# Kernel tuning notes

Measured on AMD Instinct MI355X. Metric: run time of the kernel, lower is better.

## Reference

```python
import jax, jax.numpy as jnp
import numpy as np
from functools import partial

H = 512
V = 32000


def setup_inputs() -> dict:
    key = jax.random.key(0)
    ks = jax.random.split(key, 16)
    B, Td, Te = 16, 64, 64
    s = 0.02
    inp = {
        'input_seqs': jax.random.normal(ks[0], (B, Td, H), jnp.float32),
        'input_lengths': jax.random.randint(ks[1], (B,), 1, Td + 1, jnp.int32),
        'encoder_outputs': jax.random.normal(ks[2], (B, Te, H), jnp.float32),
        'encoder_length': jax.random.randint(ks[3], (B,), 1, Te + 1, jnp.int32),
        # GRU (1 layer, batch_first): PyTorch layout W_ih (3H,H), W_hh (3H,H)
        'W_ih': jax.random.normal(ks[4], (3 * H, H), jnp.float32) * s,
        'W_hh': jax.random.normal(ks[5], (3 * H, H), jnp.float32) * s,
        'b_ih': jnp.zeros((3 * H,), jnp.float32),
        'b_hh': jnp.zeros((3 * H,), jnp.float32),
        # Attn: W: Linear(2H -> H), v: Linear(H -> 1)
        'W_attn': jax.random.normal(ks[6], (H, 2 * H), jnp.float32) * s,
        'b_attn': jnp.zeros((H,), jnp.float32),
        'v_w': jax.random.normal(ks[7], (H,), jnp.float32) * s,
        'v_b': jnp.zeros((), jnp.float32),
        # dense: Linear(2H -> H), output: Linear(H -> V)
        'W_dense': jax.random.normal(ks[8], (H, 2 * H), jnp.float32) * s,
        'b_dense': jnp.zeros((H,), jnp.float32),
        'W_out': jax.random.normal(ks[9], (V, H), jnp.float32) * s,
        'b_out': jnp.zeros((V,), jnp.float32),
    }
    return inp


def gru_forward(x, lengths, W_ih, W_hh, b_ih, b_hh):
    # Emulates pack_padded_sequence + GRU + pad_packed_sequence:
    # hidden state frozen past each sequence's length, outputs zero there.
    B, T, Hd = x.shape
    x_proj = jnp.einsum('bth,gh->btg', x, W_ih) + b_ih  # (B,T,3H)

    def step(h, inp):
        xp, t = inp  # xp: (B,3H)
        hp = h @ W_hh.T + b_hh
        xr, xz, xn = jnp.split(xp, 3, axis=-1)
        hr, hz, hn = jnp.split(hp, 3, axis=-1)
        r = jax.nn.sigmoid(xr + hr)
        z = jax.nn.sigmoid(xz + hz)
        n = jnp.tanh(xn + r * hn)
        h_new = (1.0 - z) * n + z * h
        valid = (t < lengths)[:, None]
        h_keep = jnp.where(valid, h_new, h)
        y = jnp.where(valid, h_new, 0.0)
        return h_keep, y

    h0 = jnp.zeros((B, Hd), x.dtype)
    h_last, ys = jax.lax.scan(step, h0, (x_proj.swapaxes(0, 1), jnp.arange(T)))
    return ys.swapaxes(0, 1), h_last  # (B,T,H), (B,H)


def attn_forward(enc, dec, enc_len, dec_len, W_attn, b_attn, v_w, v_b):
    B, Te, Hd = enc.shape
    Td = dec.shape[1]
    e_mask = (jnp.arange(Te) < enc_len[:, None])  # (B,Te)
    d_mask = (jnp.arange(Td) < dec_len[:, None])  # (B,Td)
    mask = (d_mask[:, :, None] & e_mask[:, None, :]).astype(enc.dtype)  # (B,Td,Te)
    # split W on the concat axis: cat(enc,dec) @ W.T = enc@We.T + dec@Wd.T
    We, Wd = W_attn[:, :Hd], W_attn[:, Hd:]
    enc_p = jnp.einsum('beh,gh->beg', enc, We)  # (B,Te,H)
    dec_p = jnp.einsum('bdh,gh->bdg', dec, Wd)  # (B,Td,H)
    m4 = mask[..., None]
    # masked-then-projected, matching enc_outputs*mask / dec_outputs*mask in torch
    score = jnp.tanh(enc_p[:, None, :, :] * m4 + dec_p[:, :, None, :] * m4 + b_attn)  # (B,Td,Te,H)
    energy = jnp.einsum('bdeh,h->bde', score, v_w) + v_b  # (B,Td,Te)
    a = jax.nn.softmax(energy, axis=2)  # softmax over ALL Te incl. masked (faithful)
    a_m = a * mask
    s = a_m.sum(axis=2)
    s = jnp.where(s == 0, 1.0, s)
    attention = a_m / s[:, :, None]  # (B,Td,Te)
    # attention is already zero where mask==0, so enc*mask == plain enc here
    context = jnp.einsum('bde,beh->bdh', attention, enc)
    return context  # dropout is identity at eval


def reference(input_seqs, input_lengths, encoder_outputs, encoder_length,
              W_ih, W_hh, b_ih, b_hh, W_attn, b_attn, v_w, v_b,
              W_dense, b_dense, W_out, b_out):
    dec_out, h_last = gru_forward(input_seqs, input_lengths, W_ih, W_hh, b_ih, b_hh)
    context = attn_forward(encoder_outputs, dec_out, encoder_length, input_lengths,
                           W_attn, b_attn, v_w, v_b)
    outputs = jnp.concatenate((dec_out, context), axis=2)  # (B,Td,2H)
    dense = jnp.tanh(jnp.einsum('bdg,hg->bdh', outputs, W_dense) + b_dense)
    logits = jnp.einsum('bdh,vh->bdv', dense, W_out) + b_out  # (B,Td,V)
    return logits, h_last[None]  # hidden: (n_layers=1, B, H)
```

## Files before the change

### kernel.cpp

```cpp
#include <hip/hip_runtime.h>
#include <stdint.h>


#define Hdim 512
#define Vdim 32000
#define Bdim 16
#define Tdim 64
#define BT   1024
#define GANG_BLOCKS 16

typedef __attribute__((ext_vector_type(8))) short bf16x8;
typedef __attribute__((ext_vector_type(4))) float f32x4;

static __device__ __forceinline__ unsigned short f2bf(float f) {
    unsigned u = __float_as_uint(f);
    u = u + 0x7FFFu + ((u >> 16) & 1u);
    return (unsigned short)(u >> 16);
}
static __device__ __forceinline__ float bf2f(unsigned short h) {
    return __uint_as_float((unsigned)h << 16);
}
static __device__ __forceinline__ float fast_tanh(float x) {
    return 2.f / (1.f + __expf(-2.f * x)) - 1.f;
}


#define U_ZERO 8320
#define U_INP  131072
#define U_WIH  196608
#define U_WAT  131072
#define U_WDE  131072
#define U_ENC  131072
#define U_SPLIT (U_INP + U_WIH + U_WAT + U_WDE + U_ENC)
#define U_WOUT 4096000
#define U_TOT  (U_ZERO + U_SPLIT + U_WOUT)

__global__ __launch_bounds__(256) void preproc_kernel(
    const float* __restrict__ input_seqs,
    const float* __restrict__ W_ih,
    const float* __restrict__ W_attn,
    const float* __restrict__ W_dense,
    const float* __restrict__ enc,
    const float* __restrict__ W_out,
    float* __restrict__ zero_base,
    unsigned short* __restrict__ inp_h, unsigned short* __restrict__ inp_l,
    unsigned short* __restrict__ Wih_h, unsigned short* __restrict__ Wih_l,
    unsigned short* __restrict__ Wat_h, unsigned short* __restrict__ Wat_l,
    unsigned short* __restrict__ Wde_h, unsigned short* __restrict__ Wde_l,
    unsigned short* __restrict__ enc_h, unsigned short* __restrict__ enc_l,
    unsigned short* __restrict__ Wout_bf)
{
    int u = blockIdx.x * 256 + threadIdx.x;
    const int stride = gridDim.x * 256;
    for (; u < U_TOT; u += stride) {
        int r = u;
        if (r < U_ZERO) {
            float4 z; z.x = 0.f; z.y = 0.f; z.z = 0.f; z.w = 0.f;
            *(float4*)(zero_base + r * 4) = z;
            continue;
        }
        r -= U_ZERO;
        if (r >= U_SPLIT) {
            int i = (r - U_SPLIT) * 4;
            float4 v = *(const float4*)(W_out + i);
            unsigned short h[4] = {f2bf(v.x), f2bf(v.y), f2bf(v.z), f2bf(v.w)};
            *(uint2*)(Wout_bf + i) = *(const uint2*)h;
            continue;
        }
        const float* src; unsigned short* hi; unsigned short* lo;
        if (r < U_INP) { src = input_seqs; hi = inp_h; lo = inp_l; }
        else { r -= U_INP;
            if (r < U_WIH) { src = W_ih; hi = Wih_h; lo = Wih_l; }
            else { r -= U_WIH;
                if (r < U_WAT) { src = W_attn; hi = Wat_h; lo = Wat_l; }
                else { r -= U_WAT;
                    if (r < U_WDE) { src = W_dense; hi = Wde_h; lo = Wde_l; }
                    else { r -= U_WDE; src = enc; hi = enc_h; lo = enc_l; }
                }
            }
        }
        int i = r * 4;
        float4 v = *(const float4*)(src + i);
        float f[4] = {v.x, v.y, v.z, v.w};
        unsigned short h[4], l[4];
#pragma unroll
        for (int k = 0; k < 4; ++k) {
            h[k] = f2bf(f[k]);
            l[k] = f2bf(f[k] - bf2f(h[k]));
        }
        *(uint2*)(hi + i) = *(const uint2*)h;
        *(uint2*)(lo + i) = *(const uint2*)l;
    }
}


struct GemmSmem {
    unsigned short AsH[128 * 40];
    unsigned short AsL[128 * 40];
    unsigned short BsH[128 * 40];
    unsigned short BsL[128 * 40];
};

static __device__ __forceinline__ void gemm_tile(
    GemmSmem& S, int m0, int n0,
    const unsigned short* __restrict__ Ah, const unsigned short* __restrict__ Al, int lda,
    const unsigned short* __restrict__ Bh, const unsigned short* __restrict__ Bl, int ldb,
    const float* __restrict__ bias,
    float* __restrict__ C, unsigned short* __restrict__ Cb, int ldc,
    int K, int act)
{
    const int tid = threadIdx.x;
    const int wave = tid >> 6, lane = tid & 63;
    const int wm = (wave >> 1) * 64, wn = (wave & 1) * 64;
    const int lrow = lane & 15, lk = (lane >> 4) * 8;

    f32x4 acc[4][4];
#pragma unroll
    for (int i = 0; i < 4; ++i)
#pragma unroll
        for (int j = 0; j < 4; ++j) acc[i][j] = (f32x4){0.f, 0.f, 0.f, 0.f};

    for (int k0 = 0; k0 < K; k0 += 32) {
#pragma unroll
        for (int i = 0; i < 2; ++i) {
            int idx = tid + i * 256;
            int rr = idx >> 2, kq = (idx & 3) * 8;
            size_t ao = (size_t)(m0 + rr) * lda + k0 + kq;
            size_t bo = (size_t)(n0 + rr) * ldb + k0 + kq;
            *(uint4*)(&S.AsH[rr * 40 + kq]) = *(const uint4*)(Ah + ao);
            *(uint4*)(&S.AsL[rr * 40 + kq]) = *(const uint4*)(Al + ao);
            *(uint4*)(&S.BsH[rr * 40 + kq]) = *(const uint4*)(Bh + bo);
            *(uint4*)(&S.BsL[rr * 40 + kq]) = *(const uint4*)(Bl + bo);
        }
        __syncthreads();
        bf16x8 ah[4], al[4], bh[4], bl[4];
#pragma unroll
        for (int i = 0; i < 4; ++i) {
            ah[i] = *(const bf16x8*)(&S.AsH[(wm + i * 16 + lrow) * 40 + lk]);
            al[i] = *(const bf16x8*)(&S.AsL[(wm + i * 16 + lrow) * 40 + lk]);
        }
#pragma unroll
        for (int j = 0; j < 4; ++j) {
            bh[j] = *(const bf16x8*)(&S.BsH[(wn + j * 16 + lrow) * 40 + lk]);
            bl[j] = *(const bf16x8*)(&S.BsL[(wn + j * 16 + lrow) * 40 + lk]);
        }
#pragma unroll
        for (int i = 0; i < 4; ++i)
#pragma unroll
            for (int j = 0; j < 4; ++j) {
                acc[i][j] = __builtin_amdgcn_mfma_f32_16x16x32_bf16(ah[i], bh[j], acc[i][j], 0, 0, 0);
                acc[i][j] = __builtin_amdgcn_mfma_f32_16x16x32_bf16(ah[i], bl[j], acc[i][j], 0, 0, 0);
                acc[i][j] = __builtin_amdgcn_mfma_f32_16x16x32_bf16(al[i], bh[j], acc[i][j], 0, 0, 0);
            }
        __syncthreads();
    }

    const int crow = m0 + wm + ((lane >> 4) * 4);
    const int ccol = n0 + wn + (lane & 15);
#pragma unroll
    for (int i = 0; i < 4; ++i) {
#pragma unroll
        for (int j = 0; j < 4; ++j) {
            int col = ccol + j * 16;
            float bv = bias[col];
#pragma unroll
            for (int rr = 0; rr < 4; ++rr) {
                int row = crow + i * 16 + rr;
                float v = acc[i][j][rr] + bv;
                if (act == 1) v = fast_tanh(v);
                if (Cb) Cb[(size_t)row * ldc + col] = f2bf(v);
                else    C [(size_t)row * ldc + col] = v;
            }
        }
    }
}

__global__ __launch_bounds__(256) void gemm_split(
    const unsigned short* __restrict__ Ah, const unsigned short* __restrict__ Al, int lda,
    const unsigned short* __restrict__ Bh, const unsigned short* __restrict__ Bl, int ldb,
    const float* __restrict__ bias,
    float* __restrict__ C, unsigned short* __restrict__ Cb, int ldc,
    int K, int act)
{
    __shared__ GemmSmem S;
    gemm_tile(S, blockIdx.y * 128, blockIdx.x * 128,
              Ah, Al, lda, Bh, Bl, ldb, bias, C, Cb, ldc, K, act);
}

__global__ __launch_bounds__(256) void gemm_split_dual(
    const unsigned short* __restrict__ A0h, const unsigned short* __restrict__ A0l,
    const unsigned short* __restrict__ B0h, const unsigned short* __restrict__ B0l,
    const float* __restrict__ bias0, float* __restrict__ C0,
    const unsigned short* __restrict__ A1h, const unsigned short* __restrict__ A1l,
    const unsigned short* __restrict__ B1h, const unsigned short* __restrict__ B1l,
    const float* __restrict__ bias1, float* __restrict__ C1)
{
    __shared__ GemmSmem S;
    const int bid = blockIdx.x;
    if (bid < 96) {
        gemm_tile(S, (bid / 12) * 128, (bid % 12) * 128,
                  A0h, A0l, Hdim, B0h, B0l, Hdim, bias0, C0, nullptr, 1536, Hdim, 0);
    } else {
        int r = bid - 96;
        gemm_tile(S, (r / 4) * 128, (r % 4) * 128,
                  A1h, A1l, Hdim, B1h, B1l, 1024, bias1, C1, nullptr, Hdim, Hdim, 0);
    }
}


__global__ __launch_bounds__(512) void gru_persistent(
    const float* __restrict__ xp,
    const float* __restrict__ Whh,
    const float* __restrict__ bhh,
    const int*   __restrict__ lengths,
    unsigned long long* __restrict__ hslots,
    unsigned short* __restrict__ cath,
    unsigned short* __restrict__ catl,
    float* __restrict__ h_last)
{
    const int bid  = blockIdx.x;
    const int b    = bid >> 4;
    const int blk  = bid & 15;
    const int tid  = threadIdx.x;
    const int wave = tid >> 6, lane = tid & 63;
    const int j0 = blk * 32 + wave * 4;
    const int k0 = lane * 8;

    __shared__ float hl[2][512];
    __shared__ unsigned short yh_buf[64][32];
    __shared__ unsigned short yl_buf[64][32];

    float w[12][8];
#pragma unroll
    for (int g = 0; g < 3; ++g)
#pragma unroll
        for (int jj = 0; jj < 4; ++jj) {
            const float* src = Whh + (size_t)(g * 512 + j0 + jj) * Hdim + k0;
            float4 a = *(const float4*)src;
            float4 bq = *(const float4*)(src + 4);
            int r = g * 4 + jj;
            w[r][0] = a.x;  w[r][1] = a.y;  w[r][2] = a.z;  w[r][3] = a.w;
            w[r][4] = bq.x; w[r][5] = bq.y; w[r][6] = bq.z; w[r][7] = bq.w;
        }

    const int j = j0 + (lane & 3);
    float bh_r = 0.f, bh_z = 0.f, bh_n = 0.f;
    if (lane < 4) {
        bh_r = bhh[j]; bh_z = bhh[512 + j]; bh_n = bhh[1024 + j];
    }
    const int len_b = lengths[b];
    float hprev = 0.f;

    const size_t PSTR = (size_t)Bdim * Hdim;
    unsigned long long* gslot = hslots + (size_t)b * Hdim;
    const float* xbase = xp + (size_t)b * Tdim * 1536;

    for (int t = 0; t < Tdim; ++t) {
        const int par = t & 1;

        float xr = 0.f, xz = 0.f, xn = 0.f;
        if (lane < 4) {
            const float* xrow = xbase + (size_t)t * 1536;
            xr = xrow[j]; xz = xrow[512 + j]; xn = xrow[1024 + j];
        }

        if (wave == 0) {
            const unsigned long long* sl = gslot + (size_t)par * PSTR + k0;
            unsigned long long v[8];
            bool ok;
            do {
#pragma unroll
                for (int q = 0; q < 8; ++q)
                    v[q] = __hip_atomic_load(sl + q, __ATOMIC_RELAXED,
                                             __HIP_MEMORY_SCOPE_AGENT);
                ok = true;
#pragma unroll
                for (int q = 0; q < 8; ++q)
                    ok = ok && ((unsigned)(v[q] >> 32) == (unsigned)t);
            } while (!ok);
#pragma unroll
            for (int q = 0; q < 8; ++q)
                hl[par][q * 64 + lane] = __uint_as_float((unsigned)v[q]);
        }
        __syncthreads();

        float hv[8];
#pragma unroll
        for (int q = 0; q < 8; ++q) hv[q] = hl[par][q * 64 + lane];

        float p[12];
#pragma unroll
        for (int r = 0; r < 12; ++r) {
            float s = 0.f;
#pragma unroll
            for (int k = 0; k < 8; ++k) s += w[r][k] * hv[k];
            p[r] = s;
        }

#pragma unroll
        for (int off = 1; off < 64; off <<= 1)
#pragma unroll
            for (int r = 0; r < 12; ++r)
                p[r] += __shfl_xor(p[r], off);

        if (lane < 4) {
            const int jj = lane;
            float hr = p[jj]     + bh_r;
            float hz = p[4 + jj] + bh_z;
            float hn = p[8 + jj] + bh_n;
            float rg = 1.f / (1.f + __expf(-(xr + hr)));
            float zg = 1.f / (1.f + __expf(-(xz + hz)));
            float ng = fast_tanh(xn + rg * hn);
            float hnew = (1.f - zg) * ng + zg * hprev;
            bool valid = t < len_b;
            float hkeep = valid ? hnew : hprev;
            hprev = hkeep;
            if (t < Tdim - 1) {
                unsigned long long pv =
                    ((unsigned long long)(unsigned)(t + 1) << 32) |
                    (unsigned long long)__float_as_uint(hkeep);
                __hip_atomic_store(gslot + (size_t)((t + 1) & 1) * PSTR + j, pv,
                                   __ATOMIC_RELAXED, __HIP_MEMORY_SCOPE_AGENT);
            } else {
                h_last[b * Hdim + j] = hkeep;
            }
            float y = valid ? hnew : 0.f;
            unsigned short yh = f2bf(y);
            yh_buf[t][wave * 4 + jj] = yh;
            yl_buf[t][wave * 4 + jj] = f2bf(y - bf2f(yh));
        }
    }

    __syncthreads();
    for (int idx = tid; idx < 64 * 16; idx += 512) {
        int t = idx >> 4, c = (idx & 15) * 2;
        size_t off = (size_t)(b * Tdim + t) * 1024 + blk * 32 + c;
        *(unsigned*)(cath + off) = *(const unsigned*)(&yh_buf[t][c]);
        *(unsigned*)(catl + off) = *(const unsigned*)(&yl_buf[t][c]);
    }
}


__global__ __launch_bounds__(256) void attn_kernel(
    const float* __restrict__ encp,
    const float* __restrict__ decp,
    const float* __restrict__ enc,
    const float* __restrict__ battn,
    const float* __restrict__ vw,
    const float* __restrict__ vb,
    const int* __restrict__ enc_len,
    const int* __restrict__ dec_len,
    unsigned short* __restrict__ cath,
    unsigned short* __restrict__ catl)
{
    const int blk = blockIdx.x;
    const int b = blk >> 6, d = blk & 63;
    const int tid = threadIdx.x;
    const size_t obase = (size_t)(b * Tdim + d) * 1024 + 512;

    if (d >= dec_len[b]) {
        for (int h = tid; h < Hdim; h += 256) { cath[obase + h] = 0; catl[obase + h] = 0; }
        return;
    }
    const int Tv = enc_len[b];

    __shared__ float dpb[512];
    __shared__ float vwl[512];
    __shared__ float part[64][4];
    __shared__ float a_lds[64];

    if (tid < 128) {
        const float4* dp4 = (const float4*)(decp + (size_t)(b * Tdim + d) * Hdim);
        float4 dv = dp4[tid];
        float4 bb = ((const float4*)battn)[tid];
        float4 r; r.x = dv.x + bb.x; r.y = dv.y + bb.y;
        r.z = dv.z + bb.z; r.w = dv.w + bb.w;
        ((float4*)dpb)[tid] = r;
        ((float4*)vwl)[tid] = ((const float4*)vw)[tid];
    }
    __syncthreads();

    const int e = tid >> 2, p = tid & 3;
    float s = 0.f;
    if (e < Tv) {
        const float4* ep4 = (const float4*)(encp + (size_t)(b * Tdim + e) * Hdim);
        const int q0 = p * 32;
        for (int q = q0; q < q0 + 32; ++q) {
            float4 ev = ep4[q];
            s += vwl[q * 4 + 0] * fast_tanh(ev.x + dpb[q * 4 + 0]);
            s += vwl[q * 4 + 1] * fast_tanh(ev.y + dpb[q * 4 + 1]);
            s += vwl[q * 4 + 2] * fast_tanh(ev.z + dpb[q * 4 + 2]);
            s += vwl[q * 4 + 3] * fast_tanh(ev.w + dpb[q * 4 + 3]);
        }
    }
    part[e][p] = s;
    __syncthreads();

    if (tid < 64) {
        const int e2 = tid;
        float en = (e2 < Tv) ? (part[e2][0] + part[e2][1] + part[e2][2] + part[e2][3] + vb[0]) : -1e30f;
        float m = en;
#pragma unroll
        for (int off = 32; off; off >>= 1) m = fmaxf(m, __shfl_xor(m, off));
        float ex = (e2 < Tv) ? __expf(en - m) : 0.f;
        float sum = ex;
#pragma unroll
        for (int off = 32; off; off >>= 1) sum += __shfl_xor(sum, off);
        a_lds[e2] = ex / sum;
    }
    __syncthreads();

    const int h = tid * 2;
    float c0 = 0.f, c1 = 0.f;
    for (int e3 = 0; e3 < Tv; ++e3) {
        float a = a_lds[e3];
        float2 ev = *(const float2*)(enc + (size_t)(b * Tdim + e3) * Hdim + h);
        c0 += a * ev.x; c1 += a * ev.y;
    }
    unsigned short h0 = f2bf(c0), h1 = f2bf(c1);
    cath[obase + h]     = h0;  catl[obase + h]     = f2bf(c0 - bf2f(h0));
    cath[obase + h + 1] = h1;  catl[obase + h + 1] = f2bf(c1 - bf2f(h1));
}


__global__ __launch_bounds__(512) void gemm_logits(
    const unsigned short* __restrict__ A,
    const unsigned short* __restrict__ B,
    const float* __restrict__ bias,
    float* __restrict__ C)
{
    const int K = Hdim;
    __shared__ unsigned short As[256 * 40];
    __shared__ unsigned short Bs[128 * 40];
    const int tid = threadIdx.x;
    const int m0 = blockIdx.y * 256, n0 = blockIdx.x * 128;
    const int wave = tid >> 6, lane = tid & 63;
    const int wm = (wave >> 1) * 64, wn = (wave & 1) * 64;
    const int lrow = lane & 15, lk = (lane >> 4) * 8;

    f32x4 acc[4][4];
#pragma unroll
    for (int i = 0; i < 4; ++i)
#pragma unroll
        for (int j = 0; j < 4; ++j) acc[i][j] = (f32x4){0.f, 0.f, 0.f, 0.f};

    for (int k0 = 0; k0 < K; k0 += 32) {
#pragma unroll
        for (int i = 0; i < 2; ++i) {
            int idx = tid + i * 512;
            int rr = idx >> 2, kq = (idx & 3) * 8;
            *(uint4*)(&As[rr * 40 + kq]) = *(const uint4*)(A + (size_t)(m0 + rr) * K + k0 + kq);
        }
        {
            int rr = tid >> 2, kq = (tid & 3) * 8;
            *(uint4*)(&Bs[rr * 40 + kq]) = *(const uint4*)(B + (size_t)(n0 + rr) * K + k0 + kq);
        }
        __syncthreads();
        bf16x8 af[4], bf[4];
#pragma unroll
        for (int i = 0; i < 4; ++i) af[i] = *(const bf16x8*)(&As[(wm + i * 16 + lrow) * 40 + lk]);
#pragma unroll
        for (int j = 0; j < 4; ++j) bf[j] = *(const bf16x8*)(&Bs[(wn + j * 16 + lrow) * 40 + lk]);
#pragma unroll
        for (int i = 0; i < 4; ++i)
#pragma unroll
            for (int j = 0; j < 4; ++j)
                acc[i][j] = __builtin_amdgcn_mfma_f32_16x16x32_bf16(af[i], bf[j], acc[i][j], 0, 0, 0);
        __syncthreads();
    }

    const int crow = m0 + wm + ((lane >> 4) * 4);
    const int ccol = n0 + wn + (lane & 15);
#pragma unroll
    for (int i = 0; i < 4; ++i) {
#pragma unroll
        for (int j = 0; j < 4; ++j) {
            int col = ccol + j * 16;
            float bv = bias[col];
#pragma unroll
            for (int rr = 0; rr < 4; ++rr) {
                int row = crow + i * 16 + rr;
                C[(size_t)row * Vdim + col] = acc[i][j][rr] + bv;
            }
        }
    }
}


extern "C" void kernel_launch(void* const* d_in, const int* in_sizes, int n_in,
                              void* d_out, int out_size, void* d_ws, size_t ws_size,
                              hipStream_t stream) {
    (void)in_sizes; (void)n_in; (void)out_size; (void)ws_size;

    const float* input_seqs  = (const float*)d_in[0];
    const int*   input_len   = (const int*)  d_in[1];
    const float* enc_out     = (const float*)d_in[2];
    const int*   enc_len     = (const int*)  d_in[3];
    const float* W_ih        = (const float*)d_in[4];
    const float* W_hh        = (const float*)d_in[5];
    const float* b_ih        = (const float*)d_in[6];
    const float* b_hh        = (const float*)d_in[7];
    const float* W_attn      = (const float*)d_in[8];
    const float* b_attn      = (const float*)d_in[9];
    const float* v_w         = (const float*)d_in[10];
    const float* v_b         = (const float*)d_in[11];
    const float* W_dense     = (const float*)d_in[12];
    const float* b_dense     = (const float*)d_in[13];
    const float* W_out       = (const float*)d_in[14];
    const float* b_out       = (const float*)d_in[15];

    float* logits = (float*)d_out;
    float* h_last = (float*)d_out + (size_t)BT * Vdim;

    float* ws    = (float*)d_ws;
    float* xp    = ws;
    float* encp  = xp   + 1572864;
    float* decp  = encp + 524288;
    unsigned long long* hslots = (unsigned long long*)(decp + 524288);
    float* zbias = (float*)(hslots + 16384);
    unsigned short* U0 = (unsigned short*)(zbias + 512);
    unsigned short* inp_h   = U0;
    unsigned short* inp_l   = U0 + 524288;
    unsigned short* Wih_h   = U0 + 1048576;
    unsigned short* Wih_l   = U0 + 1835008;
    unsigned short* Wattn_h = U0 + 2621440;
    unsigned short* Wattn_l = U0 + 3145728;
    unsigned short* Wden_h  = U0 + 3670016;
    unsigned short* Wden_l  = U0 + 4194304;
    unsigned short* enc_h   = U0 + 4718592;
    unsigned short* enc_l   = U0 + 5242880;
    unsigned short* Wout_bf = U0 + 5767168;
    unsigned short* cath = U0;
    unsigned short* catl = U0 + 1048576;
    unsigned short* dense_bf = (unsigned short*)encp;

    preproc_kernel<<<4096, 256, 0, stream>>>(
        input_seqs, W_ih, W_attn, W_dense, enc_out, W_out,
        (float*)hslots,
        inp_h, inp_l, Wih_h, Wih_l, Wattn_h, Wattn_l,
        Wden_h, Wden_l, enc_h, enc_l, Wout_bf);

    gemm_split_dual<<<128, 256, 0, stream>>>(
        inp_h, inp_l, Wih_h, Wih_l, b_ih, xp,
        enc_h, enc_l, Wattn_h, Wattn_l, zbias, encp);

    gru_persistent<<<Bdim * GANG_BLOCKS, 512, 0, stream>>>(
        xp, W_hh, b_hh, input_len, hslots, cath, catl, h_last);

    gemm_split<<<dim3(Hdim / 128, BT / 128), 256, 0, stream>>>(
        cath, catl, 1024, Wattn_h + 512, Wattn_l + 512, 1024, zbias, decp, nullptr, Hdim, Hdim, 0);

    attn_kernel<<<BT, 256, 0, stream>>>(encp, decp, enc_out, b_attn, v_w, v_b,
                                        enc_len, input_len, cath, catl);

    gemm_split<<<dim3(Hdim / 128, BT / 128), 256, 0, stream>>>(
        cath, catl, 1024, Wden_h, Wden_l, 1024, b_dense, nullptr, dense_bf, Hdim, 1024, 1);

    gemm_logits<<<dim3(Vdim / 128, BT / 256), 512, 0, stream>>>(
        dense_bf, Wout_bf, b_out, logits);
}
```

Baseline: 655.6 us.

## Shorten GRU matvec reductions and enlarge logits GEMM tile to 256x256

The GRU recurrent matvec now has 16 lanes per output row, each holding 32 weights per gate as float4. Partial sums therefore reduce over 16 lanes in 3 values instead of 64 lanes in 12 values, which cuts shuffle work on the serial critical path. A rotated chunk index spreads the shared-memory reads. Separately, the logits GEMM tile grows from 256x128 to 256x256 with 8x4 MFMA accumulators per wave, for more data reuse per block. The cost is higher register pressure and fewer blocks (500 instead of 1000).

```diff
diff --git a/kernel.cpp b/kernel.cpp
--- a/kernel.cpp
+++ b/kernel.cpp
@@ -223,29 +223,25 @@
     const int blk  = bid & 15;
     const int tid  = threadIdx.x;
     const int wave = tid >> 6, lane = tid & 63;
-    const int j0 = blk * 32 + wave * 4;
-    const int k0 = lane * 8;
+    const int g    = lane >> 4;
+    const int q    = lane & 15;
+    const int j0   = blk * 32 + wave * 4;
+    const int j    = j0 + g;
 
     __shared__ float hl[2][512];
     __shared__ unsigned short yh_buf[64][32];
     __shared__ unsigned short yl_buf[64][32];
 
-    float w[12][8];
-#pragma unroll
-    for (int g = 0; g < 3; ++g)
-#pragma unroll
-        for (int jj = 0; jj < 4; ++jj) {
-            const float* src = Whh + (size_t)(g * 512 + j0 + jj) * Hdim + k0;
-            float4 a = *(const float4*)src;
-            float4 bq = *(const float4*)(src + 4);
-            int r = g * 4 + jj;
-            w[r][0] = a.x;  w[r][1] = a.y;  w[r][2] = a.z;  w[r][3] = a.w;
-            w[r][4] = bq.x; w[r][5] = bq.y; w[r][6] = bq.z; w[r][7] = bq.w;
-        }
-
-    const int j = j0 + (lane & 3);
+    float4 w4[3][8];
+#pragma unroll
+    for (int gg = 0; gg < 3; ++gg) {
+        const float4* src = (const float4*)(Whh + (size_t)(gg * 512 + j) * Hdim + q * 32);
+#pragma unroll
+        for (int c = 0; c < 8; ++c) w4[gg][c] = src[c];
+    }
+
     float bh_r = 0.f, bh_z = 0.f, bh_n = 0.f;
-    if (lane < 4) {
+    if (q == 0) {
         bh_r = bhh[j]; bh_z = bhh[512 + j]; bh_n = bhh[1024 + j];
     }
     const int len_b = lengths[b];
@@ -259,55 +255,54 @@
         const int par = t & 1;
 
         float xr = 0.f, xz = 0.f, xn = 0.f;
-        if (lane < 4) {
+        if (q == 0) {
             const float* xrow = xbase + (size_t)t * 1536;
             xr = xrow[j]; xz = xrow[512 + j]; xn = xrow[1024 + j];
         }
 
         if (wave == 0) {
-            const unsigned long long* sl = gslot + (size_t)par * PSTR + k0;
+            const unsigned long long* sl = gslot + (size_t)par * PSTR;
             unsigned long long v[8];
             bool ok;
             do {
 #pragma unroll
-                for (int q = 0; q < 8; ++q)
-                    v[q] = __hip_atomic_load(sl + q, __ATOMIC_RELAXED,
+                for (int i = 0; i < 8; ++i)
+                    v[i] = __hip_atomic_load(sl + lane + 64 * i, __ATOMIC_RELAXED,
                                              __HIP_MEMORY_SCOPE_AGENT);
                 ok = true;
 #pragma unroll
-                for (int q = 0; q < 8; ++q)
-                    ok = ok && ((unsigned)(v[q] >> 32) == (unsigned)t);
+                for (int i = 0; i < 8; ++i)
+                    ok = ok && ((unsigned)(v[i] >> 32) == (unsigned)t);
             } while (!ok);
 #pragma unroll
-            for (int q = 0; q < 8; ++q)
-                hl[par][q * 64 + lane] = __uint_as_float((unsigned)v[q]);
+            for (int i = 0; i < 8; ++i)
+                hl[par][lane + 64 * i] = __uint_as_float((unsigned)v[i]);
         }
         __syncthreads();
 
-        float hv[8];
-#pragma unroll
-        for (int q = 0; q < 8; ++q) hv[q] = hl[par][q * 64 + lane];
-
-        float p[12];
-#pragma unroll
-        for (int r = 0; r < 12; ++r) {
-            float s = 0.f;
-#pragma unroll
-            for (int k = 0; k < 8; ++k) s += w[r][k] * hv[k];
-            p[r] = s;
-        }
-
-#pragma unroll
-        for (int off = 1; off < 64; off <<= 1)
-#pragma unroll
-            for (int r = 0; r < 12; ++r)
-                p[r] += __shfl_xor(p[r], off);
-
-        if (lane < 4) {
-            const int jj = lane;
-            float hr = p[jj]     + bh_r;
-            float hz = p[4 + jj] + bh_z;
-            float hn = p[8 + jj] + bh_n;
+        float p0 = 0.f, p1 = 0.f, p2 = 0.f;
+        const float4* h4 = (const float4*)(&hl[par][q * 32]);
+#pragma unroll
+        for (int c = 0; c < 8; ++c) {
+            int ch = (c + q) & 7;
+            float4 hv = h4[ch];
+            float4 a0 = w4[0][ch], a1 = w4[1][ch], a2 = w4[2][ch];
+            p0 += a0.x * hv.x + a0.y * hv.y + a0.z * hv.z + a0.w * hv.w;
+            p1 += a1.x * hv.x + a1.y * hv.y + a1.z * hv.z + a1.w * hv.w;
+            p2 += a2.x * hv.x + a2.y * hv.y + a2.z * hv.z + a2.w * hv.w;
+        }
+
+#pragma unroll
+        for (int off = 1; off < 16; off <<= 1) {
+            p0 += __shfl_xor(p0, off);
+            p1 += __shfl_xor(p1, off);
+            p2 += __shfl_xor(p2, off);
+        }
+
+        if (q == 0) {
+            float hr = p0 + bh_r;
+            float hz = p1 + bh_z;
+            float hn = p2 + bh_n;
             float rg = 1.f / (1.f + __expf(-(xr + hr)));
             float zg = 1.f / (1.f + __expf(-(xz + hz)));
             float ng = fast_tanh(xn + rg * hn);
@@ -326,8 +321,8 @@
             }
             float y = valid ? hnew : 0.f;
             unsigned short yh = f2bf(y);
-            yh_buf[t][wave * 4 + jj] = yh;
-            yl_buf[t][wave * 4 + jj] = f2bf(y - bf2f(yh));
+            yh_buf[t][wave * 4 + g] = yh;
+            yl_buf[t][wave * 4 + g] = f2bf(y - bf2f(yh));
         }
     }
 
@@ -431,16 +426,16 @@
 {
     const int K = Hdim;
     __shared__ unsigned short As[256 * 40];
-    __shared__ unsigned short Bs[128 * 40];
+    __shared__ unsigned short Bs[256 * 40];
     const int tid = threadIdx.x;
-    const int m0 = blockIdx.y * 256, n0 = blockIdx.x * 128;
+    const int m0 = blockIdx.y * 256, n0 = blockIdx.x * 256;
     const int wave = tid >> 6, lane = tid & 63;
-    const int wm = (wave >> 1) * 64, wn = (wave & 1) * 64;
+    const int wm = (wave >> 2) * 128, wn = (wave & 3) * 64;
     const int lrow = lane & 15, lk = (lane >> 4) * 8;
 
-    f32x4 acc[4][4];
-#pragma unroll
-    for (int i = 0; i < 4; ++i)
+    f32x4 acc[8][4];
+#pragma unroll
+    for (int i = 0; i < 8; ++i)
 #pragma unroll
         for (int j = 0; j < 4; ++j) acc[i][j] = (f32x4){0.f, 0.f, 0.f, 0.f};
 
@@ -450,19 +445,16 @@
             int idx = tid + i * 512;
             int rr = idx >> 2, kq = (idx & 3) * 8;
             *(uint4*)(&As[rr * 40 + kq]) = *(const uint4*)(A + (size_t)(m0 + rr) * K + k0 + kq);
-        }
-        {
-            int rr = tid >> 2, kq = (tid & 3) * 8;
             *(uint4*)(&Bs[rr * 40 + kq]) = *(const uint4*)(B + (size_t)(n0 + rr) * K + k0 + kq);
         }
         __syncthreads();
-        bf16x8 af[4], bf[4];
-#pragma unroll
-        for (int i = 0; i < 4; ++i) af[i] = *(const bf16x8*)(&As[(wm + i * 16 + lrow) * 40 + lk]);
+        bf16x8 af[8], bf[4];
+#pragma unroll
+        for (int i = 0; i < 8; ++i) af[i] = *(const bf16x8*)(&As[(wm + i * 16 + lrow) * 40 + lk]);
 #pragma unroll
         for (int j = 0; j < 4; ++j) bf[j] = *(const bf16x8*)(&Bs[(wn + j * 16 + lrow) * 40 + lk]);
 #pragma unroll
-        for (int i = 0; i < 4; ++i)
+        for (int i = 0; i < 8; ++i)
 #pragma unroll
             for (int j = 0; j < 4; ++j)
                 acc[i][j] = __builtin_amdgcn_mfma_f32_16x16x32_bf16(af[i], bf[j], acc[i][j], 0, 0, 0);
@@ -472,7 +464,7 @@
     const int crow = m0 + wm + ((lane >> 4) * 4);
     const int ccol = n0 + wn + (lane & 15);
 #pragma unroll
-    for (int i = 0; i < 4; ++i) {
+    for (int i = 0; i < 8; ++i) {
 #pragma unroll
         for (int j = 0; j < 4; ++j) {
             int col = ccol + j * 16;
@@ -556,6 +548,6 @@
     gemm_split<<<dim3(Hdim / 128, BT / 128), 256, 0, stream>>>(
         cath, catl, 1024, Wden_h, Wden_l, 1024, b_dense, nullptr, dense_bf, Hdim, 1024, 1);
 
-    gemm_logits<<<dim3(Vdim / 128, BT / 256), 512, 0, stream>>>(
+    gemm_logits<<<dim3(Vdim / 256, BT / 256), 512, 0, stream>>>(
         dense_bf, Wout_bf, b_out, logits);
 }
```

Result: slower. 1.394 ms (+112.6%).
